# Kernel optimization log

Hardware: AMD Instinct MI355X
Metric: run time of the kernel (lower is better)

Reference implementation:

```python
import jax, jax.numpy as jnp
import numpy as np
from jax import lax

B, N, C, T = 1024, 128, 3, 100
H = 128  # lstm hidden / feature size

def setup_inputs() -> dict:
    key = jax.random.key(0)
    ks = jax.random.split(key, 12)
    s = 0.05
    return {
        'x': jax.random.normal(ks[0], (B, N, C, T), jnp.float32),
        'conv_w': jax.random.normal(ks[1], (64, 3, 5), jnp.float32) * s,
        'conv_b': jax.random.normal(ks[2], (64,), jnp.float32) * s,
        'w_ih': jax.random.normal(ks[3], (4 * H, 64), jnp.float32) * s,
        'w_hh': jax.random.normal(ks[4], (4 * H, H), jnp.float32) * s,
        'b_ih': jax.random.normal(ks[5], (4 * H,), jnp.float32) * s,
        'b_hh': jax.random.normal(ks[6], (4 * H,), jnp.float32) * s,
        'W1': jax.random.normal(ks[7], (H, 2 * H), jnp.float32) * s,
        'W2': jax.random.normal(ks[8], (H, H), jnp.float32) * s,
        'W0': jax.random.normal(ks[9], (H, H), jnp.float32) * s,
        'ln_g': jnp.ones((H,), jnp.float32),
        'ln_b': jnp.zeros((H,), jnp.float32),
        'lin_w': jax.random.normal(ks[10], (H, H), jnp.float32) * s,
        'lin_b': jax.random.normal(ks[11], (H,), jnp.float32) * s,
    }

def _forward(x, conv_w, conv_b, w_ih, w_hh, b_ih, b_hh, W1, W2, W0, ln_g, ln_b, lin_w, lin_b):
    b, n = x.shape[0], x.shape[1]
    # --- agent encode: conv1d(3->64, k=5, pad=2) + relu on x[:,0] ---
    agent = x[:, 0]  # [B,3,T]
    h = lax.conv_general_dilated(agent, conv_w, (1,), [(2, 2)],
                                 dimension_numbers=('NCH', 'OIH', 'NCH'))
    h = jax.nn.relu(h + conv_b[None, :, None])  # [B,64,T]
    seq = jnp.transpose(h, (2, 0, 1))  # [T,B,64]
    # --- single-layer LSTM (pytorch gate order i,f,g,o) ---
    bias = b_ih + b_hh
    def step(carry, xt):
        hp, cp = carry
        gates = xt @ w_ih.T + hp @ w_hh.T + bias  # [B,4H]
        i, f, g, o = jnp.split(gates, 4, axis=-1)
        c = jax.nn.sigmoid(f) * cp + jax.nn.sigmoid(i) * jnp.tanh(g)
        hn = jax.nn.sigmoid(o) * jnp.tanh(c)
        return (hn, c), None
    init = (jnp.zeros((b, H), x.dtype), jnp.zeros((b, H), x.dtype))
    (agent_out, _), _ = lax.scan(step, init, seq)  # agent_out: [B,128]
    # NOTE: original code appends agent_out for ALL N slots (its loop bug);
    # faithful: all_vehicle_out = agent_out repeated N times.
    all_out = jnp.broadcast_to(agent_out[:, None, :], (b, n, H))  # [B,N,128]
    # --- Attention: res = W0 x0 + sum_i W2 tanh(W1 [x0; xi]) (vectorized) ---
    x0 = all_out[:, 0]           # [B,128]
    others = all_out[:, 1:]      # [B,N-1,128]
    x0b = jnp.broadcast_to(x0[:, None, :], others.shape)
    cat = jnp.concatenate([x0b, others], axis=-1)       # [B,N-1,256]
    inter = jnp.tanh(jnp.einsum('bnf,hf->bnh', cat, W1))
    inter = jnp.einsum('bnh,fh->bnf', inter, W2)        # [B,N-1,128]
    res = x0 @ W0.T + inter.sum(axis=1)                 # [B,128]
    # --- layernorm(128) ---
    mu = res.mean(-1, keepdims=True)
    var = ((res - mu) ** 2).mean(-1, keepdims=True)
    res = (res - mu) * lax.rsqrt(var + 1e-5) * ln_g + ln_b
    # --- linear(128,128) then repeat to [B,14,14,128] ---
    res = res @ lin_w.T + lin_b
    return jnp.tile(res[:, None, None, :], (1, 14, 14, 1))

def reference(x, conv_w, conv_b, w_ih, w_hh, b_ih, b_hh, W1, W2, W0, ln_g, ln_b, lin_w, lin_b):
    return _forward(x, conv_w, conv_b, w_ih, w_hh, b_ih, b_hh, W1, W2, W0, ln_g, ln_b, lin_w, lin_b)
```

## Files before the change

kernel.cpp:

```cpp
#include <hip/hip_runtime.h>
#include <math.h>


#define T_STEPS 100
#define LROW    208
#define PLANE   (16 * LROW)

#define OFF_WHI    0u
#define OFF_BIAS   393216u
#define OFF_W1CT   395264u
#define OFF_W2T    460800u
#define OFF_W0T    526336u
#define OFF_LINWT  591872u
#define OFF_XHI    657408u
#define OFF_HFIN   26871808u

typedef __attribute__((ext_vector_type(8))) _Float16 half8;
typedef __attribute__((ext_vector_type(4))) float f32x4;

__device__ __forceinline__ float frcp(float x) { return __builtin_amdgcn_rcpf(x); }
__device__ __forceinline__ float fexp2(float x) { return __builtin_amdgcn_exp2f(x); }
__device__ __forceinline__ float tanhf_fast(float x) { return 2.f * frcp(1.f + __expf(-2.f * x)) - 1.f; }

#define MF16(A, B, C) __builtin_amdgcn_mfma_f32_16x16x32_f16((A), (B), (C), 0, 0, 0)

__global__ __launch_bounds__(512)
void prep_conv_kernel(const float* __restrict__ w_ih, const float* __restrict__ w_hh,
                      const float* __restrict__ b_ih, const float* __restrict__ b_hh,
                      const float* __restrict__ W1, const float* __restrict__ W2,
                      const float* __restrict__ W0, const float* __restrict__ lin_w,
                      const float* __restrict__ x, const float* __restrict__ conv_w,
                      const float* __restrict__ conv_b, char* __restrict__ wsb) {
    __shared__ float sx[3][104];
    __shared__ float sw[960];
    __shared__ float sb[64];

    _Float16* whi  = (_Float16*)(wsb + OFF_WHI);
    float*  biasv = (float*)(wsb + OFF_BIAS);
    float*  W1cT  = (float*)(wsb + OFF_W1CT);
    float*  W2T   = (float*)(wsb + OFF_W2T);
    float*  W0T   = (float*)(wsb + OFF_W0T);
    float*  linWT = (float*)(wsb + OFF_LINWT);
    _Float16* xhi = (_Float16*)(wsb + OFF_XHI);

    const float fold[4] = {-1.4426950408889634f, -1.4426950408889634f,
                           -2.8853900817779268f, -1.4426950408889634f};

    int blk = blockIdx.x, tid = threadIdx.x;
    if (blk < 192) {
        int idx = blk * 512 + tid;
        int e = idx & 7;
        int l = (idx >> 3) & 63;
        int s = (idx >> 9) & 3;
        int rem = idx >> 11;
        int kt = rem % 6, w = rem / 6;
        int g = s * 128 + 16 * w + (l & 15);
        int k = kt * 32 + (l >> 4) * 8 + e;
        float v = (k < 64) ? w_ih[g * 64 + k] : w_hh[g * 128 + (k - 64)];
        whi[idx] = (_Float16)(v * fold[s]);
    } else if (blk == 192) {
        int s = tid >> 7;
        biasv[tid] = (b_ih[tid] + b_hh[tid]) * fold[s];
    } else if (blk < 225) {
        int idx = (blk - 193) * 512 + tid;
        int f = idx >> 7, hh = idx & 127;
        W1cT[f * 128 + hh] = W1[hh * 256 + f] + W1[hh * 256 + 128 + f];
    } else if (blk < 257) {
        int idx = (blk - 225) * 512 + tid;
        int h = idx >> 7, f = idx & 127;
        W2T[h * 128 + f] = W2[f * 128 + h];
    } else if (blk < 289) {
        int idx = (blk - 257) * 512 + tid;
        int k = idx >> 7, f = idx & 127;
        W0T[k * 128 + f] = W0[f * 128 + k];
    } else if (blk < 321) {
        int idx = (blk - 289) * 512 + tid;
        int k = idx >> 7, f = idx & 127;
        linWT[k * 128 + f] = lin_w[f * 128 + k];
    } else {
        int b = blk - 321;
        for (int i = tid; i < 312; i += 512) {
            int c = i / 104, tp = i % 104;
            int t = tp - 2;
            sx[c][tp] = (t >= 0 && t < 100) ? x[b * 38400 + c * 100 + t] : 0.f;
        }
        for (int i = tid; i < 960; i += 512) sw[i] = conv_w[i];
        if (tid < 64) sb[tid] = conv_b[tid];
        __syncthreads();

        for (int i = tid; i < 6400; i += 512) {
            int t = i >> 6, k = i & 63;
            float a = sb[k];
#pragma unroll
            for (int c = 0; c < 3; ++c)
#pragma unroll
                for (int kk = 0; kk < 5; ++kk)
                    a += sx[c][t + kk] * sw[k * 15 + c * 5 + kk];
            a = fmaxf(a, 0.f);
            xhi[t * 65536 + b * 64 + k] = (_Float16)a;
        }
    }
}

__global__ __launch_bounds__(512, 2)
void lstm_mfma(const char* __restrict__ wsro, char* __restrict__ wsb) {
    const _Float16* whi  = (const _Float16*)(wsro + OFF_WHI);
    const float*  biasv  = (const float*)(wsro + OFF_BIAS);
    const _Float16* xhi  = (const _Float16*)(wsro + OFF_XHI);
    float* hfin = (float*)(wsb + OFF_HFIN);

    __shared__ _Float16 L[2][16][LROW];

    int tid = threadIdx.x;
    int w = tid >> 6, l = tid & 63;
    int b0 = blockIdx.x * 16;

    half8 wx[2][4];
    half8 wh[4][4];
#pragma unroll
    for (int ktx = 0; ktx < 2; ++ktx)
#pragma unroll
        for (int s = 0; s < 4; ++s)
            wx[ktx][s] = *(const half8*)(whi + (((w * 6 + ktx) * 4 + s) * 64 + l) * 8);
#pragma unroll
    for (int kth = 0; kth < 4; ++kth)
#pragma unroll
        for (int s = 0; s < 4; ++s)
            wh[kth][s] = *(const half8*)(whi + (((w * 6 + 2 + kth) * 4 + s) * 64 + l) * 8);

    int jl = 16 * w + (l & 15);
    f32x4 bvec[4];
#pragma unroll
    for (int s = 0; s < 4; ++s) {
        float bv = biasv[s * 128 + jl];
        bvec[s] = (f32x4){bv, bv, bv, bv};
    }

    int arow = l & 15;
    int g16  = (l >> 4) * 16;
    uint rowbase = (uint)arow * (LROW * 2);
    uint rswz    = (uint)(arow & 7) << 4;
    int hrow0 = (l >> 4) * 4;

    int xr = tid >> 5;
    uint xw = ((uint)xr * (LROW * 2) + (uint)(tid & 31) * 4) ^ ((uint)(xr & 7) << 4);

    uint hwa[4];
#pragma unroll
    for (int r = 0; r < 4; ++r) {
        uint row = (uint)(hrow0 + r);
        hwa[r] = (row * (LROW * 2) + 128u + 2u * (uint)jl) ^ ((row & 7u) << 4);
    }

    float cst[4]  = {0.f, 0.f, 0.f, 0.f};
    float hreg[4] = {0.f, 0.f, 0.f, 0.f};

    for (int i = tid; i < 2 * PLANE; i += 512) ((_Float16*)L)[i] = (_Float16)0.f;

    size_t xoff0 = (size_t)b0 * 64 + (size_t)tid * 2;
    uint vx = *(const uint*)(xhi + xoff0);
    __syncthreads();
    *(uint*)((char*)&L[0][0][0] + xw) = vx;
    vx = *(const uint*)(xhi + xoff0 + 65536);
    __syncthreads();

    for (int t = 0; t < T_STEPS; ++t) {
        int p = t & 1;
        const char* ph = (const char*)&L[p][0][0];
        char* qh = (char*)&L[p ^ 1][0][0];

        if (t < T_STEPS - 1) {
            *(uint*)(qh + xw) = vx;
            int tn = (t + 2 < T_STEPS) ? t + 2 : T_STEPS - 1;
            vx = *(const uint*)(xhi + xoff0 + (size_t)tn * 65536);
        }

        half8 ax0 = *(const half8*)(ph + ((rowbase + 0u   + g16) ^ rswz));
        half8 ax1 = *(const half8*)(ph + ((rowbase + 64u  + g16) ^ rswz));
        half8 ah0 = *(const half8*)(ph + ((rowbase + 128u + g16) ^ rswz));
        half8 ah1 = *(const half8*)(ph + ((rowbase + 192u + g16) ^ rswz));
        half8 ah2 = *(const half8*)(ph + ((rowbase + 256u + g16) ^ rswz));
        half8 ah3 = *(const half8*)(ph + ((rowbase + 320u + g16) ^ rswz));

        f32x4 acc[4];
#pragma unroll
        for (int s = 0; s < 4; ++s) acc[s] = MF16(ax0, wx[0][s], bvec[s]);
#pragma unroll
        for (int s = 0; s < 4; ++s) acc[s] = MF16(ax1, wx[1][s], acc[s]);
#pragma unroll
        for (int s = 0; s < 4; ++s) acc[s] = MF16(ah0, wh[0][s], acc[s]);
#pragma unroll
        for (int s = 0; s < 4; ++s) acc[s] = MF16(ah1, wh[1][s], acc[s]);
#pragma unroll
        for (int s = 0; s < 4; ++s) acc[s] = MF16(ah2, wh[2][s], acc[s]);
#pragma unroll
        for (int s = 0; s < 4; ++s) acc[s] = MF16(ah3, wh[3][s], acc[s]);

#pragma unroll
        for (int r = 0; r < 4; ++r) {
            float Ei = fexp2(acc[0][r]);
            float Ef = fexp2(acc[1][r]);
            float Eg = fexp2(acc[2][r]);
            float Eo = fexp2(acc[3][r]);
            float rf  = frcp(1.f + Ef);
            float rig = frcp((1.f + Ei) * (1.f + Eg));
            cst[r] = rf * cst[r] + (1.f - Eg) * rig;
            float Ec = fexp2(cst[r] * -2.8853900817779268f);
            float roc = frcp((1.f + Eo) * (1.f + Ec));
            hreg[r] = (1.f - Ec) * roc;
        }

        if (t < T_STEPS - 1) {
#pragma unroll
            for (int r = 0; r < 4; ++r)
                *(_Float16*)(qh + hwa[r]) = (_Float16)hreg[r];
            __syncthreads();
        }
    }

#pragma unroll
    for (int r = 0; r < 4; ++r)
        hfin[(size_t)(b0 + hrow0 + r) * 128 + jl] = hreg[r];
}

__global__ __launch_bounds__(128) void post_kernel(const char* __restrict__ wsb,
                                                   const float* __restrict__ ln_g,
                                                   const float* __restrict__ ln_b,
                                                   const float* __restrict__ lin_b,
                                                   float* __restrict__ out) {
    const float* hfinal = (const float*)(wsb + OFF_HFIN);
    const float* W1cT   = (const float*)(wsb + OFF_W1CT);
    const float* W2T    = (const float*)(wsb + OFF_W2T);
    const float* W0T    = (const float*)(wsb + OFF_W0T);
    const float* linWT  = (const float*)(wsb + OFF_LINWT);

    __shared__ float sh[128], su[128], sres[128], so_[128], spart[4];
    int b = blockIdx.x, f = threadIdx.x;

    sh[f] = hfinal[(size_t)b * 128 + f];
    __syncthreads();

    float acc = 0.f;
#pragma unroll 4
    for (int k = 0; k < 128; ++k) acc += W1cT[k * 128 + f] * sh[k];
    su[f] = tanhf_fast(acc);
    __syncthreads();

    float v = 0.f, r0 = 0.f;
#pragma unroll 4
    for (int k = 0; k < 128; ++k) {
        v  += W2T[k * 128 + f] * su[k];
        r0 += W0T[k * 128 + f] * sh[k];
    }
    float res = r0 + 127.f * v;

    int lane = f & 63, wid = f >> 6;
    float s = res;
#pragma unroll
    for (int off = 32; off > 0; off >>= 1) s += __shfl_down(s, off);
    if (lane == 0) spart[wid] = s;
    __syncthreads();
    float mu = (spart[0] + spart[1]) * (1.f / 128.f);
    float d = res - mu;
    float s2 = d * d;
#pragma unroll
    for (int off = 32; off > 0; off >>= 1) s2 += __shfl_down(s2, off);
    if (lane == 0) spart[2 + wid] = s2;
    __syncthreads();
    float var = (spart[2] + spart[3]) * (1.f / 128.f);
    float rn = d * rsqrtf(var + 1e-5f) * ln_g[f] + ln_b[f];
    sres[f] = rn;
    __syncthreads();

    float o = lin_b[f];
#pragma unroll 4
    for (int k = 0; k < 128; ++k) o += linWT[k * 128 + f] * sres[k];
    so_[f] = o;
    __syncthreads();

    float4 val = *(const float4*)&so_[(f & 31) << 2];
    float4* op4 = (float4*)(out + (size_t)b * 25088);
#pragma unroll 7
    for (int i = 0; i < 49; ++i) op4[i * 128 + f] = val;
}

extern "C" void kernel_launch(void* const* d_in, const int* in_sizes, int n_in,
                              void* d_out, int out_size, void* d_ws, size_t ws_size,
                              hipStream_t stream) {
    const float* x      = (const float*)d_in[0];
    const float* conv_w = (const float*)d_in[1];
    const float* conv_b = (const float*)d_in[2];
    const float* w_ih   = (const float*)d_in[3];
    const float* w_hh   = (const float*)d_in[4];
    const float* b_ih   = (const float*)d_in[5];
    const float* b_hh   = (const float*)d_in[6];
    const float* W1     = (const float*)d_in[7];
    const float* W2     = (const float*)d_in[8];
    const float* W0     = (const float*)d_in[9];
    const float* ln_g   = (const float*)d_in[10];
    const float* ln_b   = (const float*)d_in[11];
    const float* lin_w  = (const float*)d_in[12];
    const float* lin_b  = (const float*)d_in[13];
    char* wsb  = (char*)d_ws;
    float* out = (float*)d_out;

    prep_conv_kernel<<<dim3(1345), dim3(512), 0, stream>>>(w_ih, w_hh, b_ih, b_hh,
                                                           W1, W2, W0, lin_w,
                                                           x, conv_w, conv_b, wsb);
    lstm_mfma<<<dim3(64), dim3(512), 0, stream>>>(wsb, wsb);
    post_kernel<<<dim3(1024), dim3(128), 0, stream>>>(wsb, ln_g, ln_b, lin_b, out);
}
```

Before: 148.4 us.

## Load LSTM input fragments directly from global into registers, shrink LDS to h only

The LSTM step no longer stages the conv output x_t through shared memory. Each lane now loads its MFMA A-fragment for x straight from global memory into registers, two steps ahead, and the shared buffer holds only the hidden state. The loop is unrolled by two with register ping-pong, so the x-part MFMAs can be issued before the h reads and the per-step LDS store of x goes away. The trade-off is 16-byte strided global loads per lane that may not be fully hidden on the serial recurrence, plus higher register use.

```diff
diff --git a/kernel.cpp b/kernel.cpp
--- a/kernel.cpp
+++ b/kernel.cpp
@@ -3,8 +3,6 @@
 
 
 #define T_STEPS 100
-#define LROW    208
-#define PLANE   (16 * LROW)
 
 #define OFF_WHI    0u
 #define OFF_BIAS   393216u
@@ -109,7 +107,7 @@
     const _Float16* xhi  = (const _Float16*)(wsro + OFF_XHI);
     float* hfin = (float*)(wsb + OFF_HFIN);
 
-    __shared__ _Float16 L[2][16][LROW];
+    __shared__ _Float16 H[2][16][128];
 
     int tid = threadIdx.x;
     int w = tid >> 6, l = tid & 63;
@@ -137,86 +135,86 @@
     }
 
     int arow = l & 15;
-    int g16  = (l >> 4) * 16;
-    uint rowbase = (uint)arow * (LROW * 2);
-    uint rswz    = (uint)(arow & 7) << 4;
+    uint g16b = (uint)(l >> 4) << 4;
+    uint rswz = (uint)(arow & 7) << 4;
     int hrow0 = (l >> 4) * 4;
 
-    int xr = tid >> 5;
-    uint xw = ((uint)xr * (LROW * 2) + (uint)(tid & 31) * 4) ^ ((uint)(xr & 7) << 4);
-
-    uint hwa[4];
+    char* hb = (char*)&H[0][0][0];
+
+    const uint ha0 = ((uint)arow * 256u + 0u   + g16b) ^ rswz;
+    const uint ha1 = ((uint)arow * 256u + 64u  + g16b) ^ rswz;
+    const uint ha2 = ((uint)arow * 256u + 128u + g16b) ^ rswz;
+    const uint ha3 = ((uint)arow * 256u + 192u + g16b) ^ rswz;
+    uint hw_[4];
 #pragma unroll
     for (int r = 0; r < 4; ++r) {
         uint row = (uint)(hrow0 + r);
-        hwa[r] = (row * (LROW * 2) + 128u + 2u * (uint)jl) ^ ((row & 7u) << 4);
-    }
+        hw_[r] = (row * 256u + 2u * (uint)jl) ^ ((row & 7u) << 4);
+    }
+
+    const _Float16* xb = xhi + (size_t)(b0 + arow) * 64 + (size_t)((l >> 4) * 8);
 
     float cst[4]  = {0.f, 0.f, 0.f, 0.f};
     float hreg[4] = {0.f, 0.f, 0.f, 0.f};
 
-    for (int i = tid; i < 2 * PLANE; i += 512) ((_Float16*)L)[i] = (_Float16)0.f;
-
-    size_t xoff0 = (size_t)b0 * 64 + (size_t)tid * 2;
-    uint vx = *(const uint*)(xhi + xoff0);
-    __syncthreads();
-    *(uint*)((char*)&L[0][0][0] + xw) = vx;
-    vx = *(const uint*)(xhi + xoff0 + 65536);
-    __syncthreads();
-
-    for (int t = 0; t < T_STEPS; ++t) {
-        int p = t & 1;
-        const char* ph = (const char*)&L[p][0][0];
-        char* qh = (char*)&L[p ^ 1][0][0];
-
-        if (t < T_STEPS - 1) {
-            *(uint*)(qh + xw) = vx;
-            int tn = (t + 2 < T_STEPS) ? t + 2 : T_STEPS - 1;
-            vx = *(const uint*)(xhi + xoff0 + (size_t)tn * 65536);
-        }
-
-        half8 ax0 = *(const half8*)(ph + ((rowbase + 0u   + g16) ^ rswz));
-        half8 ax1 = *(const half8*)(ph + ((rowbase + 64u  + g16) ^ rswz));
-        half8 ah0 = *(const half8*)(ph + ((rowbase + 128u + g16) ^ rswz));
-        half8 ah1 = *(const half8*)(ph + ((rowbase + 192u + g16) ^ rswz));
-        half8 ah2 = *(const half8*)(ph + ((rowbase + 256u + g16) ^ rswz));
-        half8 ah3 = *(const half8*)(ph + ((rowbase + 320u + g16) ^ rswz));
-
-        f32x4 acc[4];
-#pragma unroll
-        for (int s = 0; s < 4; ++s) acc[s] = MF16(ax0, wx[0][s], bvec[s]);
-#pragma unroll
-        for (int s = 0; s < 4; ++s) acc[s] = MF16(ax1, wx[1][s], acc[s]);
-#pragma unroll
-        for (int s = 0; s < 4; ++s) acc[s] = MF16(ah0, wh[0][s], acc[s]);
-#pragma unroll
-        for (int s = 0; s < 4; ++s) acc[s] = MF16(ah1, wh[1][s], acc[s]);
-#pragma unroll
-        for (int s = 0; s < 4; ++s) acc[s] = MF16(ah2, wh[2][s], acc[s]);
-#pragma unroll
-        for (int s = 0; s < 4; ++s) acc[s] = MF16(ah3, wh[3][s], acc[s]);
-
-#pragma unroll
-        for (int r = 0; r < 4; ++r) {
-            float Ei = fexp2(acc[0][r]);
-            float Ef = fexp2(acc[1][r]);
-            float Eg = fexp2(acc[2][r]);
-            float Eo = fexp2(acc[3][r]);
-            float rf  = frcp(1.f + Ef);
-            float rig = frcp((1.f + Ei) * (1.f + Eg));
-            cst[r] = rf * cst[r] + (1.f - Eg) * rig;
-            float Ec = fexp2(cst[r] * -2.8853900817779268f);
-            float roc = frcp((1.f + Eo) * (1.f + Ec));
-            hreg[r] = (1.f - Ec) * roc;
-        }
-
-        if (t < T_STEPS - 1) {
-#pragma unroll
-            for (int r = 0; r < 4; ++r)
-                *(_Float16*)(qh + hwa[r]) = (_Float16)hreg[r];
-            __syncthreads();
-        }
-    }
+    for (int i = tid; i < 2048; i += 512) ((uint*)hb)[i] = 0u;
+
+    half8 ga0 = *(const half8*)(xb);
+    half8 ga1 = *(const half8*)(xb + 32);
+    half8 gb0 = *(const half8*)(xb + 65536);
+    half8 gb1 = *(const half8*)(xb + 65536 + 32);
+    __syncthreads();
+
+#define PWISE(R)                                                              \
+    { float Ei = fexp2(acc[0][R]);                                           \
+      float Ef = fexp2(acc[1][R]);                                           \
+      float Eg = fexp2(acc[2][R]);                                           \
+      float Eo = fexp2(acc[3][R]);                                           \
+      float rf  = frcp(1.f + Ef);                                            \
+      float rig = frcp((1.f + Ei) * (1.f + Eg));                             \
+      cst[R] = rf * cst[R] + (1.f - Eg) * rig;                                \
+      float Ec = fexp2(cst[R] * -2.8853900817779268f);                        \
+      float roc = frcp((1.f + Eo) * (1.f + Ec));                              \
+      hreg[R] = (1.f - Ec) * roc; }
+
+#define XSTEP(GX0, GX1, POFF, QOFF, TNEXT, DOWRITE)                           \
+    { f32x4 acc[4];                                                           \
+      _Pragma("unroll")                                                       \
+      for (int s = 0; s < 4; ++s) acc[s] = MF16(GX0, wx[0][s], bvec[s]);      \
+      _Pragma("unroll")                                                       \
+      for (int s = 0; s < 4; ++s) acc[s] = MF16(GX1, wx[1][s], acc[s]);       \
+      GX0 = *(const half8*)(xb + (size_t)(TNEXT) * 65536);                    \
+      GX1 = *(const half8*)(xb + (size_t)(TNEXT) * 65536 + 32);               \
+      const char* hp = hb + (POFF);                                           \
+      half8 ah0 = *(const half8*)(hp + ha0);                                  \
+      half8 ah1 = *(const half8*)(hp + ha1);                                  \
+      half8 ah2 = *(const half8*)(hp + ha2);                                  \
+      half8 ah3 = *(const half8*)(hp + ha3);                                  \
+      _Pragma("unroll")                                                       \
+      for (int s = 0; s < 4; ++s) acc[s] = MF16(ah0, wh[0][s], acc[s]);       \
+      _Pragma("unroll")                                                       \
+      for (int s = 0; s < 4; ++s) acc[s] = MF16(ah1, wh[1][s], acc[s]);       \
+      _Pragma("unroll")                                                       \
+      for (int s = 0; s < 4; ++s) acc[s] = MF16(ah2, wh[2][s], acc[s]);       \
+      _Pragma("unroll")                                                       \
+      for (int s = 0; s < 4; ++s) acc[s] = MF16(ah3, wh[3][s], acc[s]);       \
+      PWISE(0) PWISE(1) PWISE(2) PWISE(3)                                     \
+      if (DOWRITE) {                                                          \
+          char* hq = hb + (QOFF);                                             \
+          _Pragma("unroll")                                                   \
+          for (int r = 0; r < 4; ++r)                                         \
+              *(_Float16*)(hq + hw_[r]) = (_Float16)hreg[r];                  \
+          __syncthreads();                                                    \
+      } }
+
+    for (int tt = 0; tt < T_STEPS; tt += 2) {
+        int tn0 = (tt + 2 < T_STEPS) ? tt + 2 : T_STEPS - 1;
+        XSTEP(ga0, ga1, 0, 4096, tn0, true)
+        int tn1 = (tt + 3 < T_STEPS) ? tt + 3 : T_STEPS - 1;
+        XSTEP(gb0, gb1, 4096, 0, tn1, (tt < T_STEPS - 2))
+    }
+#undef XSTEP
+#undef PWISE
 
 #pragma unroll
     for (int r = 0; r < 4; ++r)
```

After: 162.9 us. 1.1x slower.
